# Kernel optimization log

Hardware: AMD Instinct MI355X
Metric: run time of the kernel (lower is better)

The kernel has to match this reference:

```python
import jax, jax.numpy as jnp
import numpy as np

N_ITER = 2
N_NEIGHBOR = 8
NEG = -9.0e15


def _rel_transform(emb, rel, W_rel):
    # emb: [..., d] neighbor embeddings, rel: [...] relation ids.
    # Original applies tanh(W_r @ e) to entries whose relation == r (all entries
    # are covered since rel in [0, n_relation)). Small fixed loop over relations.
    out = jnp.zeros_like(emb)
    for r in range(W_rel.shape[0]):
        y = jnp.tanh(jnp.einsum('...d,ed->...e', emb, W_rel[r]))  # Linear(bias=False): x @ W.T
        out = out + jnp.where((rel == r)[..., None], y, jnp.zeros_like(y))
    return out


def _masked_softmax(s):
    s = jnp.where(s == 0, NEG, s)
    return jax.nn.softmax(s, axis=-1)


def _forward(user_indices, item_indices, entity_emb, W_rel, adj_entity,
             adj_relation, items_clicked, num_clicked, labels_table, offset):
    bs = user_indices.shape[0]
    dim = entity_emb.shape[1]
    n_old = adj_entity.shape[1]

    # user embedding = sum of clicked item embeddings * 1/num_clicked
    hist = items_clicked[user_indices]                              # [bs, H]
    user_emb = entity_emb[hist].sum(axis=1) * (1.0 / num_clicked[user_indices])[:, None]
    user_emb4 = user_emb.reshape(bs, 1, 1, dim)

    seeds = item_indices.reshape(bs, 1, 1)
    entities = [seeds]
    entities_emb = [entity_emb[seeds]]                              # [bs,1,1,d]
    scores_us = []
    for i in range(N_ITER):
        nbr_e = adj_entity[entities[i]].reshape(bs, -1, n_old)      # [bs,N,64]
        nbr_r = adj_relation[entities[i]].reshape(bs, -1, n_old)
        nbr_emb = _rel_transform(entity_emb[nbr_e], nbr_r, W_rel)   # [bs,N,64,d]
        s = jnp.mean(user_emb4 * nbr_emb, axis=-1)                  # [bs,N,64]
        s = _masked_softmax(s)
        s_top, ids = jax.lax.top_k(s, N_NEIGHBOR)                   # sort desc + slice
        s_top = _masked_softmax(s_top)
        scores_us.append(s_top)                                     # [bs,N,K]
        nbr_e = jnp.take_along_axis(nbr_e, ids, axis=-1)
        nbr_r = jnp.take_along_axis(nbr_r, ids, axis=-1)
        nbr_emb = _rel_transform(entity_emb[nbr_e], nbr_r, W_rel)   # [bs,N,K,d]
        entities.append(nbr_e)
        entities_emb.append(nbr_emb)

    # label propagation setup (dense stand-in for the TF hash table; 0.5 = missing)
    entity_labels, reset_masks = [], []
    holdout = None
    for ent in entities:
        ent2 = ent.reshape(bs, -1)
        concat = user_indices[:, None] * offset + ent2
        if holdout is None:
            holdout = concat
        lab = labels_table[user_indices[:, None], ent2]
        holdout_mask = (holdout - concat) != 0
        reset_mask = (lab != 0.5) & holdout_mask
        lab = jnp.where(holdout_mask, lab, jnp.asarray(0.5, lab.dtype))
        entity_labels.append(lab)
        reset_masks.append(reset_mask)
    reset_masks = reset_masks[:-1]

    for i in range(N_ITER):
        next_emb, next_lab = [], []
        for hop in range(N_ITER - i):
            agg = jnp.mean(scores_us[hop][..., None] * entities_emb[hop + 1],
                           axis=2, keepdims=True).reshape(entities_emb[hop].shape)
            lab_agg = jnp.sum(scores_us[hop] *
                              entity_labels[hop + 1].reshape(bs, -1, N_NEIGHBOR), axis=-1)
            lab_out = jnp.where(reset_masks[hop], entity_labels[hop], lab_agg)
            act = jnp.tanh if i == N_ITER - 1 else jax.nn.relu
            next_emb.append(act(agg + entities_emb[hop]))
            next_lab.append(lab_out)
        entities_emb, entity_labels = next_emb, next_lab

    pred_labels = entity_labels[0].reshape(bs)
    item_out = entities_emb[0].reshape(bs, dim)
    scores = jax.nn.sigmoid(jnp.sum(user_emb * item_out, axis=1))
    pred_labels = jax.nn.sigmoid(pred_labels - 0.5)
    return scores, pred_labels


def setup_inputs() -> dict:
    key = jax.random.key(0)
    ks = jax.random.split(key, 10)
    n_user, n_entity, n_rel, dim = 1024, 50000, 8, 64
    n_old, hist, bs = 64, 50, 1024
    entity_emb = jax.random.normal(ks[0], (n_entity + 1, dim), jnp.float32) * 0.1
    entity_emb = entity_emb.at[-1].set(0.0)  # padding_idx row
    W_rel = jax.random.normal(ks[1], (n_rel, dim, dim), jnp.float32) / np.float32(np.sqrt(dim))
    adj_entity = jax.random.randint(ks[2], (n_entity + 1, n_old), 0, n_entity)
    adj_relation = jax.random.randint(ks[3], (n_entity + 1, n_old), 0, n_rel)
    items_clicked = jax.random.randint(ks[4], (n_user, hist), 0, n_entity + 1)
    num_clicked = jax.random.uniform(ks[5], (n_user,), jnp.float32, 1.0, float(hist))
    labels_table = jax.random.choice(ks[6], jnp.array([0.0, 0.5, 1.0], jnp.float32),
                                     (n_user, n_entity + 1))
    user_indices = jax.random.randint(ks[7], (bs,), 0, n_user)
    item_indices = jax.random.randint(ks[8], (bs,), 0, n_entity)
    return dict(user_indices=user_indices, item_indices=item_indices,
                entity_emb=entity_emb, W_rel=W_rel, adj_entity=adj_entity,
                adj_relation=adj_relation, items_clicked=items_clicked,
                num_clicked=num_clicked, labels_table=labels_table,
                offset=n_entity + 1)


def reference(user_indices, item_indices, entity_emb, W_rel, adj_entity,
              adj_relation, items_clicked, num_clicked, labels_table, offset):
    return _forward(user_indices, item_indices, entity_emb, W_rel, adj_entity,
                    adj_relation, items_clicked, num_clicked, labels_table, offset)
```

## Files before the change

### kernel.cpp

```cpp
#include <hip/hip_runtime.h>
#include <math.h>

#define NEGV -9000000000000000.0f
#define WPB 16
#define NTHR 1024

struct LdsW {
  float4 w[8 * 16 * 64];
  float xb[WPB][64];
};

__device__ __forceinline__ float wave_sum(float v) {
#pragma unroll
  for (int m = 32; m; m >>= 1) v += __shfl_xor(v, m, 64);
  return v;
}

__device__ __forceinline__ int rl(int v, int l) {
  return __builtin_amdgcn_readlane(v, l);
}

__device__ __forceinline__ void stage_W(float4* wl, const float* __restrict__ W) {
  const float4* Wg = (const float4*)W;
  for (int f = threadIdx.x; f < 8192; f += NTHR) {
    float4 v = Wg[f];
    int r = f >> 10, e = (f >> 4) & 63, k = f & 15;
    wl[(((r << 4) + k) << 6) + e] = v;
  }
  __syncthreads();
}

__device__ __forceinline__ void load_xu_hi(const float* __restrict__ emb, int nb,
                                           float4 xu[8]) {
  const float4* xg = (const float4*)(emb + ((size_t)nb << 6) + 32);
#pragma unroll
  for (int j = 0; j < 8; ++j) xu[j] = xg[j];
}

__device__ __forceinline__ void load_xu_full(const float* __restrict__ emb, int nb,
                                             float4 xu[16]) {
  const float4* xg = (const float4*)(emb + ((size_t)nb << 6));
#pragma unroll
  for (int j = 0; j < 16; ++j) xu[j] = xg[j];
}

__device__ __forceinline__ float transform_pre(const float4 xu[16], int r, int lane,
                                               const float4* wl) {
  const float4* wr = wl + (r << 10) + lane;
  float acc = 0.f;
#pragma unroll
  for (int k = 0; k < 16; ++k) {
    float4 w = wr[k << 6];
    acc = fmaf(w.x, xu[k].x, acc);
    acc = fmaf(w.y, xu[k].y, acc);
    acc = fmaf(w.z, xu[k].z, acc);
    acc = fmaf(w.w, xu[k].w, acc);
  }
  return tanhf(acc);
}

__device__ __forceinline__ void score_step(int pos, int lane, const float4* wl,
                                           float* xbuf, const float* __restrict__ emb,
                                           int srt_r, int srt_nb, int order, float u_e,
                                           float4 wv[16], int& rcur, float& xv,
                                           float& s_mine, const float4 xu_cur[8],
                                           float4 xu_next[8]) {
  int r = rl(srt_r, pos);
  if (r != rcur) {
    const float4* wr = wl + (r << 10) + lane;
#pragma unroll
    for (int k = 0; k < 16; ++k) wv[k] = wr[k << 6];
#pragma unroll
    for (int k = 0; k < 16; ++k)
      asm volatile("" : "+v"(wv[k].x), "+v"(wv[k].y), "+v"(wv[k].z), "+v"(wv[k].w));
    rcur = r;
  }
  int nbn = (pos < 63) ? rl(srt_nb, pos + 1) : 0;
  __builtin_amdgcn_wave_barrier();
  if (lane < 32) xbuf[lane] = xv;
  __builtin_amdgcn_wave_barrier();
  float xnext = 0.f;
  if (pos < 63 && lane < 32) xnext = emb[((size_t)nbn << 6) + lane];
  asm volatile("s_waitcnt lgkmcnt(0)" ::: "memory");
  __builtin_amdgcn_wave_barrier();
  if (pos < 63) load_xu_hi(emb, nbn, xu_next);
  float acc = 0.f;
#pragma unroll
  for (int k = 0; k < 8; ++k) {
    float4 x = *(const float4*)(xbuf + 4 * k);
    acc = fmaf(wv[k].x, x.x, acc);
    acc = fmaf(wv[k].y, x.y, acc);
    acc = fmaf(wv[k].z, x.z, acc);
    acc = fmaf(wv[k].w, x.w, acc);
  }
#pragma unroll
  for (int k = 8; k < 16; ++k) {
    acc = fmaf(wv[k].x, xu_cur[k - 8].x, acc);
    acc = fmaf(wv[k].y, xu_cur[k - 8].y, acc);
    acc = fmaf(wv[k].z, xu_cur[k - 8].z, acc);
    acc = fmaf(wv[k].w, xu_cur[k - 8].w, acc);
  }
  float y = tanhf(acc);
  float totv = wave_sum(u_e * y);
  int n = rl(order, pos);
  if (lane == n) s_mine = totv * (1.0f / 64.0f);
  xv = xnext;
}

__device__ __forceinline__ void score_select(int eid, int b, int lane,
                                             const float* __restrict__ emb,
                                             const float4* wl, float* xbuf,
                                             const int* __restrict__ adjE,
                                             const int* __restrict__ adjR,
                                             const float* __restrict__ user_emb,
                                             int& nbr, int& rel, int seli[8],
                                             float wout[8]) {
  nbr = adjE[((size_t)eid << 6) + lane];
  rel = adjR[((size_t)eid << 6) + lane];
  float u_e = user_emb[((size_t)b << 6) + lane];
  int myrank = 0, basec = 0;
  unsigned long long ltmask = (1ull << lane) - 1ull;
#pragma unroll
  for (int rr = 0; rr < 8; ++rr) {
    unsigned long long m = __ballot(rel == rr);
    if (rel == rr) myrank = basec + (int)__popcll(m & ltmask);
    basec += (int)__popcll(m);
  }
  int order = __builtin_amdgcn_ds_permute(myrank << 2, lane);
  int srt_nb = __shfl(nbr, order, 64);
  int srt_r = __shfl(rel, order, 64);

  int nb0 = rl(srt_nb, 0);
  float xv = 0.f;
  if (lane < 32) xv = emb[((size_t)nb0 << 6) + lane];
  float4 xuA[8], xuB[8];
  load_xu_hi(emb, nb0, xuA);
  float4 wv[16];
  int rcur = -1;
  float s_mine = 0.f;
  for (int pos = 0; pos < 64; pos += 2) {
    score_step(pos, lane, wl, xbuf, emb, srt_r, srt_nb, order, u_e, wv, rcur, xv,
               s_mine, xuA, xuB);
    score_step(pos + 1, lane, wl, xbuf, emb, srt_r, srt_nb, order, u_e, wv, rcur, xv,
               s_mine, xuB, xuA);
  }
  float sv = (s_mine == 0.0f) ? NEGV : s_mine;
  float mx = sv;
#pragma unroll
  for (int m = 32; m; m >>= 1) mx = fmaxf(mx, __shfl_xor(mx, m, 64));
  float p = expf(sv - mx);
  float Z = wave_sum(p);
  p /= Z;
  float v = p;
  int vi = lane;
  float selv[8];
#pragma unroll
  for (int j = 0; j < 8; ++j) {
    float bv = v;
    int bi = vi;
#pragma unroll
    for (int m = 1; m < 64; m <<= 1) {
      float ov = __shfl_xor(bv, m, 64);
      int oi = __shfl_xor(bi, m, 64);
      if (ov > bv || (ov == bv && oi < bi)) { bv = ov; bi = oi; }
    }
    selv[j] = bv;
    seli[j] = bi;
    if (lane == bi) v = -__builtin_inff();
  }
  float m8 = -__builtin_inff();
#pragma unroll
  for (int j = 0; j < 8; ++j) {
    float tt = (selv[j] == 0.f) ? NEGV : selv[j];
    selv[j] = tt;
    m8 = fmaxf(m8, tt);
  }
  float Z8 = 0.f;
#pragma unroll
  for (int j = 0; j < 8; ++j) {
    selv[j] = expf(selv[j] - m8);
    Z8 += selv[j];
  }
#pragma unroll
  for (int j = 0; j < 8; ++j) wout[j] = selv[j] / Z8;
}

__global__ __launch_bounds__(256) void k_user(const int* __restrict__ ui,
                                              const float* __restrict__ emb,
                                              const int* __restrict__ clicked,
                                              const float* __restrict__ numc, int hist,
                                              float* __restrict__ user_emb, int ntask) {
  int w = threadIdx.x >> 6, lane = threadIdx.x & 63;
  int b = blockIdx.x * 4 + w;
  if (b >= ntask) return;
  int u = ui[b];
  float acc = 0.f;
  for (int h = 0; h < hist; ++h) {
    int it = clicked[u * hist + h];
    acc += emb[((size_t)it << 6) + lane];
  }
  user_emb[((size_t)b << 6) + lane] = acc * (1.0f / numc[u]);
}

__global__ __launch_bounds__(NTHR, 4) void k_hop0_f(
    const int* __restrict__ ii, const float* __restrict__ emb,
    const float* __restrict__ W, const int* __restrict__ adjE,
    const int* __restrict__ adjR, const float* __restrict__ user_emb,
    int* __restrict__ e1, float* __restrict__ s0w, float* __restrict__ emb1,
    int ntask) {
  __shared__ LdsW S;
  stage_W(S.w, W);
  int w = threadIdx.x >> 6, lane = threadIdx.x & 63;
  int wid = blockIdx.x * WPB + w;
  int tot = gridDim.x * WPB;
  for (int t = wid; t < ntask; t += tot) {
    int eid = ii[t];
    int nbr, rel, seli[8];
    float w8[8];
    score_select(eid, t, lane, emb, S.w, S.xb[w], adjE, adjR, user_emb, nbr, rel, seli,
                 w8);
    int nbs[8], rrs[8];
#pragma unroll
    for (int j = 0; j < 8; ++j) {
      int sj = __builtin_amdgcn_readfirstlane(seli[j]);
      nbs[j] = rl(nbr, sj);
      rrs[j] = rl(rel, sj);
    }
    float4 xtA[16], xtB[16];
    load_xu_full(emb, nbs[0], xtA);
#pragma unroll
    for (int j = 0; j < 8; ++j) {
      const float4* xc = (j & 1) ? xtB : xtA;
      float4* xn = (j & 1) ? xtA : xtB;
      if (j < 7) load_xu_full(emb, nbs[j + 1], xn);
      float y = transform_pre(xc, rrs[j], lane, S.w);
      emb1[(((size_t)t * 8 + j) << 6) + lane] = y;
      if (lane == 0) {
        e1[t * 8 + j] = nbs[j];
        s0w[t * 8 + j] = w8[j];
      }
    }
  }
}

__global__ __launch_bounds__(NTHR, 4) void k_hop1_f(
    const int* __restrict__ ui, const int* __restrict__ ii, const float* __restrict__ emb,
    const float* __restrict__ W, const int* __restrict__ adjE,
    const int* __restrict__ adjR, const float* __restrict__ labels, int np1,
    const float* __restrict__ user_emb, const int* __restrict__ e1,
    const float* __restrict__ emb1, float* __restrict__ emb1p,
    float* __restrict__ lab1p, int ntask) {
  __shared__ LdsW S;
  stage_W(S.w, W);
  int w = threadIdx.x >> 6, lane = threadIdx.x & 63;
  int wid = blockIdx.x * WPB + w;
  int tot = gridDim.x * WPB;
  for (int bj = wid; bj < ntask; bj += tot) {
    int b = bj >> 3;
    int u = ui[b];
    int item = ii[b];
    int eid = e1[bj];
    int nbr, rel, seli[8];
    float w8[8];
    score_select(eid, b, lane, emb, S.w, S.xb[w], adjE, adjR, user_emb, nbr, rel, seli,
                 w8);
    int nbs[8], rrs[8];
#pragma unroll
    for (int k = 0; k < 8; ++k) {
      int sk = __builtin_amdgcn_readfirstlane(seli[k]);
      nbs[k] = rl(nbr, sk);
      rrs[k] = rl(rel, sk);
    }
    float4 xtA[16], xtB[16];
    load_xu_full(emb, nbs[0], xtA);
    float agg = 0.f, labagg = 0.f;
#pragma unroll
    for (int k = 0; k < 8; ++k) {
      const float4* xc = (k & 1) ? xtB : xtA;
      float4* xn = (k & 1) ? xtA : xtB;
      if (k < 7) load_xu_full(emb, nbs[k + 1], xn);
      float y = transform_pre(xc, rrs[k], lane, S.w);
      agg = fmaf(w8[k], y, agg);
      float raw2 = labels[(size_t)u * np1 + nbs[k]];
      float lab2 = (nbs[k] != item) ? raw2 : 0.5f;
      labagg = fmaf(w8[k], lab2, labagg);
    }
    float base = emb1[((size_t)bj << 6) + lane];
    emb1p[((size_t)bj << 6) + lane] = fmaxf(fmaf(agg, 0.125f, base), 0.f);
    if (lane == 0) {
      float raw1 = labels[(size_t)u * np1 + eid];
      bool hm = (eid != item);
      float l1 = hm ? raw1 : 0.5f;
      bool reset1 = (raw1 != 0.5f) && hm;
      lab1p[bj] = reset1 ? l1 : labagg;
    }
  }
}

__global__ __launch_bounds__(256) void k_final(const int* __restrict__ ii,
                                               const float* __restrict__ emb,
                                               const float* __restrict__ user_emb,
                                               const float* __restrict__ s0,
                                               const float* __restrict__ emb1,
                                               const float* __restrict__ emb1p,
                                               const float* __restrict__ lab1p,
                                               float* __restrict__ out, int bs) {
  int w = threadIdx.x >> 6, lane = threadIdx.x & 63;
  int b = blockIdx.x * 4 + w;
  if (b >= bs) return;
  int item = ii[b];
  float ue = user_emb[((size_t)b << 6) + lane];
  float agg = 0.f, aggp = 0.f, lab = 0.f;
#pragma unroll
  for (int j = 0; j < 8; ++j) {
    float s = s0[b * 8 + j];
    agg = fmaf(s, emb1[(((size_t)b * 8 + j) << 6) + lane], agg);
    aggp = fmaf(s, emb1p[(((size_t)b * 8 + j) << 6) + lane], aggp);
    lab = fmaf(s, lab1p[b * 8 + j], lab);
  }
  float e0 = emb[((size_t)item << 6) + lane];
  float h = fmaxf(fmaf(agg, 0.125f, e0), 0.f);
  float h2 = tanhf(fmaf(aggp, 0.125f, h));
  float dot = wave_sum(ue * h2);
  if (lane == 0) {
    out[b] = 1.f / (1.f + expf(-dot));
    out[bs + b] = 1.f / (1.f + expf(-(lab - 0.5f)));
  }
}

extern "C" void kernel_launch(void* const* d_in, const int* in_sizes, int n_in, void* d_out,
                              int out_size, void* d_ws, size_t ws_size, hipStream_t stream) {
  const int* ui = (const int*)d_in[0];
  const int* ii = (const int*)d_in[1];
  const float* emb = (const float*)d_in[2];
  const float* W = (const float*)d_in[3];
  const int* adjE = (const int*)d_in[4];
  const int* adjR = (const int*)d_in[5];
  const int* clicked = (const int*)d_in[6];
  const float* numc = (const float*)d_in[7];
  const float* labels = (const float*)d_in[8];

  int bs = in_sizes[0];
  int np1 = in_sizes[2] / 64;
  int nuser = in_sizes[7];
  int hist = in_sizes[6] / nuser;

  float* user_emb = (float*)d_ws;
  float* s0w = user_emb + (size_t)bs * 64;
  int* e1 = (int*)(s0w + (size_t)bs * 8);
  float* emb1 = (float*)(e1 + (size_t)bs * 8);
  float* emb1p = emb1 + (size_t)bs * 8 * 64;
  float* lab1p = emb1p + (size_t)bs * 8 * 64;

  int nt0 = bs;
  int nt1 = bs * 8;

  k_user<<<(nt0 + 3) / 4, 256, 0, stream>>>(ui, emb, clicked, numc, hist, user_emb, nt0);
  k_hop0_f<<<256, NTHR, 0, stream>>>(ii, emb, W, adjE, adjR, user_emb, e1, s0w, emb1,
                                     nt0);
  k_hop1_f<<<256, NTHR, 0, stream>>>(ui, ii, emb, W, adjE, adjR, labels, np1, user_emb,
                                     e1, emb1, emb1p, lab1p, nt1);
  k_final<<<(nt0 + 3) / 4, 256, 0, stream>>>(ii, emb, user_emb, s0w, emb1, emb1p, lab1p,
                                             (float*)d_out, bs);
}
```

Measured before the change: 261.2 us.

## Pre-transpose relation weights once into global memory instead of per-block LDS staging

Adds a small prep kernel that writes the relation weight matrices once, in the transposed layout, into workspace. The hop kernels then read weights from global memory (L2/cache) instead of each block staging 128KB into LDS, which shrinks LDS use to a per-wave scratch buffer. Grid size doubles, tasks are assigned across blocks in a strided order, and the x-prefetch switches to a single buffer reloaded in place. The trade-off is cache traffic on every relation switch in exchange for removing the per-block staging cost and the occupancy limit set by LDS.

```diff
diff --git a/kernel.cpp b/kernel.cpp
--- a/kernel.cpp
+++ b/kernel.cpp
@@ -5,11 +5,6 @@
 #define WPB 16
 #define NTHR 1024
 
-struct LdsW {
-  float4 w[8 * 16 * 64];
-  float xb[WPB][64];
-};
-
 __device__ __forceinline__ float wave_sum(float v) {
 #pragma unroll
   for (int m = 32; m; m >>= 1) v += __shfl_xor(v, m, 64);
@@ -20,14 +15,12 @@
   return __builtin_amdgcn_readlane(v, l);
 }
 
-__device__ __forceinline__ void stage_W(float4* wl, const float* __restrict__ W) {
-  const float4* Wg = (const float4*)W;
-  for (int f = threadIdx.x; f < 8192; f += NTHR) {
-    float4 v = Wg[f];
-    int r = f >> 10, e = (f >> 4) & 63, k = f & 15;
-    wl[(((r << 4) + k) << 6) + e] = v;
-  }
-  __syncthreads();
+__global__ __launch_bounds__(NTHR) void k_prep(const float* __restrict__ W,
+                                               float4* __restrict__ wp) {
+  int f = blockIdx.x * NTHR + threadIdx.x;
+  float4 v = ((const float4*)W)[f];
+  int r = f >> 10, e = (f >> 4) & 63, k = f & 15;
+  wp[(((r << 4) + k) << 6) + e] = v;
 }
 
 __device__ __forceinline__ void load_xu_hi(const float* __restrict__ emb, int nb,
@@ -45,8 +38,8 @@
 }
 
 __device__ __forceinline__ float transform_pre(const float4 xu[16], int r, int lane,
-                                               const float4* wl) {
-  const float4* wr = wl + (r << 10) + lane;
+                                               const float4* __restrict__ wp) {
+  const float4* wr = wp + (r << 10) + lane;
   float acc = 0.f;
 #pragma unroll
   for (int k = 0; k < 16; ++k) {
@@ -59,15 +52,15 @@
   return tanhf(acc);
 }
 
-__device__ __forceinline__ void score_step(int pos, int lane, const float4* wl,
-                                           float* xbuf, const float* __restrict__ emb,
-                                           int srt_r, int srt_nb, int order, float u_e,
+__device__ __forceinline__ void score_step(int pos, int lane,
+                                           const float4* __restrict__ wp, float* xbuf,
+                                           const float* __restrict__ emb, int srt_r,
+                                           int srt_nb, int order, float u_e,
                                            float4 wv[16], int& rcur, float& xv,
-                                           float& s_mine, const float4 xu_cur[8],
-                                           float4 xu_next[8]) {
+                                           float& s_mine, float4 xu[8]) {
   int r = rl(srt_r, pos);
   if (r != rcur) {
-    const float4* wr = wl + (r << 10) + lane;
+    const float4* wr = wp + (r << 10) + lane;
 #pragma unroll
     for (int k = 0; k < 16; ++k) wv[k] = wr[k << 6];
 #pragma unroll
@@ -77,13 +70,12 @@
   }
   int nbn = (pos < 63) ? rl(srt_nb, pos + 1) : 0;
   __builtin_amdgcn_wave_barrier();
-  if (lane < 32) xbuf[lane] = xv;
+  xbuf[lane] = xv;
   __builtin_amdgcn_wave_barrier();
   float xnext = 0.f;
-  if (pos < 63 && lane < 32) xnext = emb[((size_t)nbn << 6) + lane];
+  if (pos < 63) xnext = emb[((size_t)nbn << 6) + lane];
   asm volatile("s_waitcnt lgkmcnt(0)" ::: "memory");
   __builtin_amdgcn_wave_barrier();
-  if (pos < 63) load_xu_hi(emb, nbn, xu_next);
   float acc = 0.f;
 #pragma unroll
   for (int k = 0; k < 8; ++k) {
@@ -95,11 +87,12 @@
   }
 #pragma unroll
   for (int k = 8; k < 16; ++k) {
-    acc = fmaf(wv[k].x, xu_cur[k - 8].x, acc);
-    acc = fmaf(wv[k].y, xu_cur[k - 8].y, acc);
-    acc = fmaf(wv[k].z, xu_cur[k - 8].z, acc);
-    acc = fmaf(wv[k].w, xu_cur[k - 8].w, acc);
-  }
+    acc = fmaf(wv[k].x, xu[k - 8].x, acc);
+    acc = fmaf(wv[k].y, xu[k - 8].y, acc);
+    acc = fmaf(wv[k].z, xu[k - 8].z, acc);
+    acc = fmaf(wv[k].w, xu[k - 8].w, acc);
+  }
+  if (pos < 63) load_xu_hi(emb, nbn, xu);
   float y = tanhf(acc);
   float totv = wave_sum(u_e * y);
   int n = rl(order, pos);
@@ -109,7 +102,7 @@
 
 __device__ __forceinline__ void score_select(int eid, int b, int lane,
                                              const float* __restrict__ emb,
-                                             const float4* wl, float* xbuf,
+                                             const float4* __restrict__ wp, float* xbuf,
                                              const int* __restrict__ adjE,
                                              const int* __restrict__ adjR,
                                              const float* __restrict__ user_emb,
@@ -131,19 +124,15 @@
   int srt_r = __shfl(rel, order, 64);
 
   int nb0 = rl(srt_nb, 0);
-  float xv = 0.f;
-  if (lane < 32) xv = emb[((size_t)nb0 << 6) + lane];
-  float4 xuA[8], xuB[8];
-  load_xu_hi(emb, nb0, xuA);
+  float xv = emb[((size_t)nb0 << 6) + lane];
+  float4 xu[8];
+  load_xu_hi(emb, nb0, xu);
   float4 wv[16];
   int rcur = -1;
   float s_mine = 0.f;
-  for (int pos = 0; pos < 64; pos += 2) {
-    score_step(pos, lane, wl, xbuf, emb, srt_r, srt_nb, order, u_e, wv, rcur, xv,
-               s_mine, xuA, xuB);
-    score_step(pos + 1, lane, wl, xbuf, emb, srt_r, srt_nb, order, u_e, wv, rcur, xv,
-               s_mine, xuB, xuA);
-  }
+  for (int pos = 0; pos < 64; ++pos)
+    score_step(pos, lane, wp, xbuf, emb, srt_r, srt_nb, order, u_e, wv, rcur, xv,
+               s_mine, xu);
   float sv = (s_mine == 0.0f) ? NEGV : s_mine;
   float mx = sv;
 #pragma unroll
@@ -204,20 +193,18 @@
 
 __global__ __launch_bounds__(NTHR, 4) void k_hop0_f(
     const int* __restrict__ ii, const float* __restrict__ emb,
-    const float* __restrict__ W, const int* __restrict__ adjE,
+    const float4* __restrict__ wp, const int* __restrict__ adjE,
     const int* __restrict__ adjR, const float* __restrict__ user_emb,
     int* __restrict__ e1, float* __restrict__ s0w, float* __restrict__ emb1,
     int ntask) {
-  __shared__ LdsW S;
-  stage_W(S.w, W);
+  __shared__ __align__(16) float xb[WPB][64];
   int w = threadIdx.x >> 6, lane = threadIdx.x & 63;
-  int wid = blockIdx.x * WPB + w;
   int tot = gridDim.x * WPB;
-  for (int t = wid; t < ntask; t += tot) {
+  for (int t = blockIdx.x + gridDim.x * w; t < ntask; t += tot) {
     int eid = ii[t];
     int nbr, rel, seli[8];
     float w8[8];
-    score_select(eid, t, lane, emb, S.w, S.xb[w], adjE, adjR, user_emb, nbr, rel, seli,
+    score_select(eid, t, lane, emb, wp, xb[w], adjE, adjR, user_emb, nbr, rel, seli,
                  w8);
     int nbs[8], rrs[8];
 #pragma unroll
@@ -233,7 +220,7 @@
       const float4* xc = (j & 1) ? xtB : xtA;
       float4* xn = (j & 1) ? xtA : xtB;
       if (j < 7) load_xu_full(emb, nbs[j + 1], xn);
-      float y = transform_pre(xc, rrs[j], lane, S.w);
+      float y = transform_pre(xc, rrs[j], lane, wp);
       emb1[(((size_t)t * 8 + j) << 6) + lane] = y;
       if (lane == 0) {
         e1[t * 8 + j] = nbs[j];
@@ -245,24 +232,22 @@
 
 __global__ __launch_bounds__(NTHR, 4) void k_hop1_f(
     const int* __restrict__ ui, const int* __restrict__ ii, const float* __restrict__ emb,
-    const float* __restrict__ W, const int* __restrict__ adjE,
+    const float4* __restrict__ wp, const int* __restrict__ adjE,
     const int* __restrict__ adjR, const float* __restrict__ labels, int np1,
     const float* __restrict__ user_emb, const int* __restrict__ e1,
     const float* __restrict__ emb1, float* __restrict__ emb1p,
     float* __restrict__ lab1p, int ntask) {
-  __shared__ LdsW S;
-  stage_W(S.w, W);
+  __shared__ __align__(16) float xb[WPB][64];
   int w = threadIdx.x >> 6, lane = threadIdx.x & 63;
-  int wid = blockIdx.x * WPB + w;
   int tot = gridDim.x * WPB;
-  for (int bj = wid; bj < ntask; bj += tot) {
+  for (int bj = blockIdx.x + gridDim.x * w; bj < ntask; bj += tot) {
     int b = bj >> 3;
     int u = ui[b];
     int item = ii[b];
     int eid = e1[bj];
     int nbr, rel, seli[8];
     float w8[8];
-    score_select(eid, b, lane, emb, S.w, S.xb[w], adjE, adjR, user_emb, nbr, rel, seli,
+    score_select(eid, b, lane, emb, wp, xb[w], adjE, adjR, user_emb, nbr, rel, seli,
                  w8);
     int nbs[8], rrs[8];
 #pragma unroll
@@ -279,7 +264,7 @@
       const float4* xc = (k & 1) ? xtB : xtA;
       float4* xn = (k & 1) ? xtA : xtB;
       if (k < 7) load_xu_full(emb, nbs[k + 1], xn);
-      float y = transform_pre(xc, rrs[k], lane, S.w);
+      float y = transform_pre(xc, rrs[k], lane, wp);
       agg = fmaf(w8[k], y, agg);
       float raw2 = labels[(size_t)u * np1 + nbs[k]];
       float lab2 = (nbs[k] != item) ? raw2 : 0.5f;
@@ -345,7 +330,8 @@
   int nuser = in_sizes[7];
   int hist = in_sizes[6] / nuser;
 
-  float* user_emb = (float*)d_ws;
+  float4* wp = (float4*)d_ws;
+  float* user_emb = (float*)(wp + 8192);
   float* s0w = user_emb + (size_t)bs * 64;
   int* e1 = (int*)(s0w + (size_t)bs * 8);
   float* emb1 = (float*)(e1 + (size_t)bs * 8);
@@ -355,10 +341,11 @@
   int nt0 = bs;
   int nt1 = bs * 8;
 
+  k_prep<<<8, NTHR, 0, stream>>>(W, wp);
   k_user<<<(nt0 + 3) / 4, 256, 0, stream>>>(ui, emb, clicked, numc, hist, user_emb, nt0);
-  k_hop0_f<<<256, NTHR, 0, stream>>>(ii, emb, W, adjE, adjR, user_emb, e1, s0w, emb1,
+  k_hop0_f<<<512, NTHR, 0, stream>>>(ii, emb, wp, adjE, adjR, user_emb, e1, s0w, emb1,
                                      nt0);
-  k_hop1_f<<<256, NTHR, 0, stream>>>(ui, ii, emb, W, adjE, adjR, labels, np1, user_emb,
+  k_hop1_f<<<512, NTHR, 0, stream>>>(ui, ii, emb, wp, adjE, adjR, labels, np1, user_emb,
                                      e1, emb1, emb1p, lab1p, nt1);
   k_final<<<(nt0 + 3) / 4, 256, 0, stream>>>(ii, emb, user_emb, s0w, emb1, emb1p, lab1p,
                                              (float*)d_out, bs);
```

New measurement: 316.2 us. 1.21x slower.

## Single-buffer high-half neighbor prefetch and stripe task assignment across blocks

Applied to the files above, without the earlier changes.

The score loop drops the A/B double buffer for the upper half of each neighbor embedding. It now uses one 8-float4 register array, refilled with the next neighbor's data right after the current FMAs consume it, and the loop is no longer unrolled by two. The low-half staging to LDS now loads and writes all 64 lanes instead of only lanes 0-31. The hop0 task index is also remapped so consecutive tasks go to different blocks rather than to waves of the same block. This is meant to cut vector register pressure and improve occupancy or load balance, at the cost of less latency hiding between the prefetch and its use.

```diff
diff --git a/kernel.cpp b/kernel.cpp
--- a/kernel.cpp
+++ b/kernel.cpp
@@ -63,8 +63,7 @@
                                            float* xbuf, const float* __restrict__ emb,
                                            int srt_r, int srt_nb, int order, float u_e,
                                            float4 wv[16], int& rcur, float& xv,
-                                           float& s_mine, const float4 xu_cur[8],
-                                           float4 xu_next[8]) {
+                                           float& s_mine, float4 xu[8]) {
   int r = rl(srt_r, pos);
   if (r != rcur) {
     const float4* wr = wl + (r << 10) + lane;
@@ -77,13 +76,12 @@
   }
   int nbn = (pos < 63) ? rl(srt_nb, pos + 1) : 0;
   __builtin_amdgcn_wave_barrier();
-  if (lane < 32) xbuf[lane] = xv;
+  xbuf[lane] = xv;
   __builtin_amdgcn_wave_barrier();
   float xnext = 0.f;
-  if (pos < 63 && lane < 32) xnext = emb[((size_t)nbn << 6) + lane];
+  if (pos < 63) xnext = emb[((size_t)nbn << 6) + lane];
   asm volatile("s_waitcnt lgkmcnt(0)" ::: "memory");
   __builtin_amdgcn_wave_barrier();
-  if (pos < 63) load_xu_hi(emb, nbn, xu_next);
   float acc = 0.f;
 #pragma unroll
   for (int k = 0; k < 8; ++k) {
@@ -95,11 +93,12 @@
   }
 #pragma unroll
   for (int k = 8; k < 16; ++k) {
-    acc = fmaf(wv[k].x, xu_cur[k - 8].x, acc);
-    acc = fmaf(wv[k].y, xu_cur[k - 8].y, acc);
-    acc = fmaf(wv[k].z, xu_cur[k - 8].z, acc);
-    acc = fmaf(wv[k].w, xu_cur[k - 8].w, acc);
-  }
+    acc = fmaf(wv[k].x, xu[k - 8].x, acc);
+    acc = fmaf(wv[k].y, xu[k - 8].y, acc);
+    acc = fmaf(wv[k].z, xu[k - 8].z, acc);
+    acc = fmaf(wv[k].w, xu[k - 8].w, acc);
+  }
+  if (pos < 63) load_xu_hi(emb, nbn, xu);
   float y = tanhf(acc);
   float totv = wave_sum(u_e * y);
   int n = rl(order, pos);
@@ -131,19 +130,15 @@
   int srt_r = __shfl(rel, order, 64);
 
   int nb0 = rl(srt_nb, 0);
-  float xv = 0.f;
-  if (lane < 32) xv = emb[((size_t)nb0 << 6) + lane];
-  float4 xuA[8], xuB[8];
-  load_xu_hi(emb, nb0, xuA);
+  float xv = emb[((size_t)nb0 << 6) + lane];
+  float4 xu[8];
+  load_xu_hi(emb, nb0, xu);
   float4 wv[16];
   int rcur = -1;
   float s_mine = 0.f;
-  for (int pos = 0; pos < 64; pos += 2) {
+  for (int pos = 0; pos < 64; ++pos)
     score_step(pos, lane, wl, xbuf, emb, srt_r, srt_nb, order, u_e, wv, rcur, xv,
-               s_mine, xuA, xuB);
-    score_step(pos + 1, lane, wl, xbuf, emb, srt_r, srt_nb, order, u_e, wv, rcur, xv,
-               s_mine, xuB, xuA);
-  }
+               s_mine, xu);
   float sv = (s_mine == 0.0f) ? NEGV : s_mine;
   float mx = sv;
 #pragma unroll
@@ -211,9 +206,8 @@
   __shared__ LdsW S;
   stage_W(S.w, W);
   int w = threadIdx.x >> 6, lane = threadIdx.x & 63;
-  int wid = blockIdx.x * WPB + w;
   int tot = gridDim.x * WPB;
-  for (int t = wid; t < ntask; t += tot) {
+  for (int t = blockIdx.x + gridDim.x * w; t < ntask; t += tot) {
     int eid = ii[t];
     int nbr, rel, seli[8];
     float w8[8];
```

Measured after the change: 213.7 us. 18.2% less time.
